# Performance work log

Hardware: AMD Instinct MI355X
Metric: run time of the kernel (lower is better)

Reference implementation:

```python
import jax, jax.numpy as jnp
import numpy as np

DIM = 1024
HEADS = 16
DIM_HEAD = 64
INNER = HEADS * DIM_HEAD  # 1024
EPS = 1e-5


def _layernorm(x, gamma, beta):
    mu = jnp.mean(x, axis=-1, keepdims=True)
    var = jnp.var(x, axis=-1, keepdims=True)
    return (x - mu) * jax.lax.rsqrt(var + EPS) * gamma + beta


def setup_inputs() -> dict:
    key = jax.random.key(0)
    ks = jax.random.split(key, 7)
    b, m, n = 8, 4096, 64
    x = jax.random.normal(ks[0], (b, m, DIM), dtype=jnp.float32)
    latents = jax.random.normal(ks[1], (b, n, DIM), dtype=jnp.float32)
    # LayerNorm params (torch default: weight=1, bias=0; randomize slightly)
    g1 = jnp.ones((DIM,), jnp.float32)
    b1 = jnp.zeros((DIM,), jnp.float32)
    g2 = jnp.ones((DIM,), jnp.float32)
    b2 = jnp.zeros((DIM,), jnp.float32)
    s = 1.0 / np.sqrt(DIM)
    Wq = jax.random.normal(ks[2], (DIM, INNER), jnp.float32) * s   # [in, out]
    Wkv = jax.random.normal(ks[3], (DIM, 2 * INNER), jnp.float32) * s
    Wo = jax.random.normal(ks[4], (INNER, DIM), jnp.float32) * s
    return {"x": x, "latents": latents, "g1": g1, "b1": b1,
            "g2": g2, "b2": b2, "Wq": Wq, "Wkv": Wkv, "Wo": Wo}


def reference(x, latents, g1, b1, g2, b2, Wq, Wkv, Wo):
    b, n, _ = latents.shape
    h, d = HEADS, DIM_HEAD
    scale = d ** -0.5

    xn = _layernorm(x, g1, b1)
    ln = _layernorm(latents, g2, b2)

    q = ln @ Wq                              # [b, n, inner]
    kv_input = jnp.concatenate((xn, ln), axis=1)  # [b, m+n, dim]
    kv = kv_input @ Wkv                      # [b, m+n, 2*inner]
    k, v = jnp.split(kv, 2, axis=-1)
    s_kv = kv_input.shape[1]

    q = q.reshape(b, n, h, d).transpose(0, 2, 1, 3)      # bhnd
    k = k.reshape(b, s_kv, h, d).transpose(0, 2, 1, 3)   # bhsd
    v = v.reshape(b, s_kv, h, d).transpose(0, 2, 1, 3)   # bhsd

    # double-scaling trick: (q*scale) @ (k*scale)^T  => effective 1/d
    weight = jnp.einsum('bhnd,bhsd->bhns', q * scale, k * scale)
    weight = jax.nn.softmax(weight.astype(jnp.float32), axis=-1).astype(weight.dtype)
    out = jnp.einsum('bhns,bhsd->bhnd', weight, v)
    out = out.transpose(0, 2, 1, 3).reshape(b, n, h * d)
    return out @ Wo
```

## Files before the change

### kernel.cpp

```cpp
#include <hip/hip_runtime.h>

typedef __bf16 bf16;
typedef bf16 bf16x4_t __attribute__((ext_vector_type(4)));
typedef bf16 bf16x8_t __attribute__((ext_vector_type(8)));
typedef float f32x4_t __attribute__((ext_vector_type(4)));

#define DI __device__ __forceinline__

DI void gload_lds16(const void* g, void* l) {
  __builtin_amdgcn_global_load_lds((const __attribute__((address_space(1))) void*)g,
                                   (__attribute__((address_space(3))) void*)l, 16, 0, 0);
}

DI f32x4_t mfma16(bf16x8_t a, bf16x8_t b, f32x4_t c) {
  return __builtin_amdgcn_mfma_f32_16x16x32_bf16(a, b, c, 0, 0, 0);
}

DI unsigned short bfbits(float f) {
  bf16 h = (bf16)f;
  return __builtin_bit_cast(unsigned short, h);
}

__global__ __launch_bounds__(256) void prep_all(const float* __restrict__ x,
                                                const float* __restrict__ lat,
                                                const float* __restrict__ g1,
                                                const float* __restrict__ b1,
                                                const float* __restrict__ g2,
                                                const float* __restrict__ b2,
                                                const float* __restrict__ Wq,
                                                const float* __restrict__ Wkv,
                                                const float* __restrict__ Wo,
                                                bf16* __restrict__ kv_in,
                                                bf16* __restrict__ lnq,
                                                bf16* __restrict__ Wq_t,
                                                bf16* __restrict__ Wkv_t,
                                                bf16* __restrict__ Wo_t) {
  const int bid = blockIdx.x;
  const int t = threadIdx.x;
  if (bid < 8320) {
    const int wv = t >> 6, l = t & 63;
    const int row = bid * 4 + wv;
    const float* in;
    const float* gamma;
    const float* beta;
    size_t orow;
    bool dual = false;
    int lrow = 0;
    if (row < 32768) {
      in = x + (size_t)row * 1024;
      gamma = g1; beta = b1;
      orow = (size_t)(row >> 12) * 4160 + (row & 4095);
    } else {
      const int r = row - 32768;
      in = lat + (size_t)r * 1024;
      gamma = g2; beta = b2;
      orow = (size_t)(r >> 6) * 4160 + 4096 + (r & 63);
      dual = true;
      lrow = r;
    }
    float4 v[4];
    float s = 0.f, q = 0.f;
#pragma unroll
    for (int i = 0; i < 4; ++i) {
      v[i] = ((const float4*)in)[i * 64 + l];
      s += v[i].x + v[i].y + v[i].z + v[i].w;
      q += v[i].x * v[i].x + v[i].y * v[i].y + v[i].z * v[i].z + v[i].w * v[i].w;
    }
#pragma unroll
    for (int off = 1; off < 64; off <<= 1) {
      s += __shfl_xor(s, off);
      q += __shfl_xor(q, off);
    }
    const float mu = s * (1.f / 1024.f);
    const float var = q * (1.f / 1024.f) - mu * mu;
    const float rs = rsqrtf(var + 1e-5f);
#pragma unroll
    for (int i = 0; i < 4; ++i) {
      const float4 gv = ((const float4*)gamma)[i * 64 + l];
      const float4 bv = ((const float4*)beta)[i * 64 + l];
      bf16x4_t o;
      o[0] = (bf16)((v[i].x - mu) * rs * gv.x + bv.x);
      o[1] = (bf16)((v[i].y - mu) * rs * gv.y + bv.y);
      o[2] = (bf16)((v[i].z - mu) * rs * gv.z + bv.z);
      o[3] = (bf16)((v[i].w - mu) * rs * gv.w + bv.w);
      *(bf16x4_t*)(kv_in + orow * 1024 + i * 256 + l * 4) = o;
      if (dual) *(bf16x4_t*)(lnq + (size_t)lrow * 1024 + i * 256 + l * 4) = o;
    }
  } else {
    __shared__ float tile[32][33];
    const int b2i = bid - 8320;
    const float* W;
    bf16* Wt;
    int C, t0;
    if (b2i < 1024)      { W = Wq;  Wt = Wq_t;  C = 1024; t0 = b2i; }
    else if (b2i < 3072) { W = Wkv; Wt = Wkv_t; C = 2048; t0 = b2i - 1024; }
    else                 { W = Wo;  Wt = Wo_t;  C = 1024; t0 = b2i - 3072; }
    const int R = 1024;
    const int ntx = C >> 5;
    const int c0 = (t0 % ntx) * 32, r0 = (t0 / ntx) * 32;
    const int tx = t & 31, ty = t >> 5;
#pragma unroll
    for (int j = 0; j < 4; ++j)
      tile[ty + j * 8][tx] = W[(size_t)(r0 + ty + j * 8) * C + c0 + tx];
    __syncthreads();
#pragma unroll
    for (int j = 0; j < 4; ++j)
      Wt[(size_t)(c0 + ty + j * 8) * R + r0 + tx] = (bf16)tile[tx][ty + j * 8];
  }
}

__global__ __launch_bounds__(256) void gemm_bt_sk(const bf16* __restrict__ A,
                                                  const bf16* __restrict__ Bt,
                                                  float* __restrict__ Cf) {
  __shared__ bf16 As[128 * 32];
  __shared__ bf16 Bs[128 * 32];
  const int tid = threadIdx.x;
  const int w = tid >> 6, l = tid & 63;
  const int lg = l >> 4, lr = l & 15;
  const int m0 = blockIdx.y * 128, n0 = blockIdx.x * 128;
  const int kbase = blockIdx.z * 256;
  const int wm = w >> 1, wn = w & 1;
  const int K = 1024, N = 1024;

  f32x4_t acc[4][4];
#pragma unroll
  for (int i = 0; i < 4; ++i)
#pragma unroll
    for (int j = 0; j < 4; ++j)
      acc[i][j] = f32x4_t{0.f, 0.f, 0.f, 0.f};

  for (int kt = 0; kt < 8; ++kt) {
    const int k0 = kbase + kt * 32;
#pragma unroll
    for (int j = 0; j < 2; ++j) {
      const int rb = j * 64 + w * 16;
      const int r = rb + (l >> 2);
      const int c = (l & 3) * 8;
      gload_lds16(A + (size_t)(m0 + r) * K + k0 + c, &As[rb * 32]);
      gload_lds16(Bt + (size_t)(n0 + r) * K + k0 + c, &Bs[rb * 32]);
    }
    __syncthreads();
    bf16x8_t af[4], bfr[4];
#pragma unroll
    for (int i = 0; i < 4; ++i) {
      af[i] = *(const bf16x8_t*)&As[(wm * 64 + i * 16 + lr) * 32 + lg * 8];
      bfr[i] = *(const bf16x8_t*)&Bs[(wn * 64 + i * 16 + lr) * 32 + lg * 8];
    }
#pragma unroll
    for (int mf = 0; mf < 4; ++mf)
#pragma unroll
      for (int nf = 0; nf < 4; ++nf)
        acc[mf][nf] = mfma16(af[mf], bfr[nf], acc[mf][nf]);
    __syncthreads();
  }

#pragma unroll
  for (int mf = 0; mf < 4; ++mf)
#pragma unroll
    for (int r = 0; r < 4; ++r) {
      const int grow = m0 + wm * 64 + mf * 16 + 4 * lg + r;
#pragma unroll
      for (int nf = 0; nf < 4; ++nf) {
        const int gcol = n0 + wn * 64 + nf * 16 + lr;
        unsafeAtomicAdd(&Cf[(size_t)grow * N + gcol], acc[mf][nf][r]);
      }
    }
}

__global__ __launch_bounds__(512, 2) void gemm256_kv(const bf16* __restrict__ Akv,
                                                     const bf16* __restrict__ Aq,
                                                     const bf16* __restrict__ BtKV,
                                                     const bf16* __restrict__ BtQ,
                                                     bf16* __restrict__ Kout,
                                                     bf16* __restrict__ Vout,
                                                     bf16* __restrict__ Qout) {
  extern __shared__ char lds[];
  const int tid = threadIdx.x;
  const int w = tid >> 6, l = tid & 63;
  const int lr = l & 15, lg = l >> 4;
  const int wr = w >> 2, wc = w & 3;

  const int cpx = gridDim.x >> 3;
  const int swz = (blockIdx.x & 7) * cpx + (blockIdx.x >> 3);
  const bool isQ = swz >= 1040;
  const bf16* Ap;
  const bf16* Bp;
  int m0, n0;
  if (!isQ) {
    m0 = (swz >> 3) << 8;
    n0 = (swz & 7) << 8;
    Ap = Akv; Bp = BtKV;
  } else {
    const int qi = swz - 1040;
    m0 = (qi >> 2) << 8;
    n0 = (qi & 3) << 8;
    Ap = Aq; Bp = BtQ;
  }

  auto stage = [&](const bf16* __restrict__ G, int row0, int k0, char* base, int half) {
#pragma unroll
    for (int j = 0; j < 2; ++j) {
      const int r0 = half * 128 + (w * 2 + j) * 8;
      const int row = r0 + (l >> 3);
      const int col = ((l & 7) ^ (l >> 3)) * 8;
      gload_lds16(G + (size_t)(row0 + row) * 1024 + k0 + col, base + r0 * 128);
    }
  };
  auto rdA = [&](char* base, int mf, int ks) -> bf16x8_t {
    const int row = wr * 128 + mf * 16 + lr;
    int byte = row * 128 + (ks * 32 + lg * 8) * 2;
    byte ^= (row & 7) << 4;
    return *(const bf16x8_t*)(base + byte);
  };
  auto rdB = [&](char* base, int nf, int ks) -> bf16x8_t {
    const int row = wc * 64 + nf * 16 + lr;
    int byte = row * 128 + (ks * 32 + lg * 8) * 2;
    byte ^= (row & 7) << 4;
    return *(const bf16x8_t*)(base + byte);
  };

  f32x4_t acc[8][4];
#pragma unroll
  for (int i = 0; i < 8; ++i)
#pragma unroll
    for (int j = 0; j < 4; ++j)
      acc[i][j] = f32x4_t{0.f, 0.f, 0.f, 0.f};

  const int NK = 16;

  stage(Ap, m0, 0, lds, 0);
  stage(Ap, m0, 0, lds, 1);
  stage(Bp, n0, 0, lds + 32768, 0);
  stage(Bp, n0, 0, lds + 32768, 1);
  stage(Ap, m0, 64, lds + 65536, 0);
  stage(Ap, m0, 64, lds + 65536, 1);
  asm volatile("s_waitcnt vmcnt(4)" ::: "memory");
  __builtin_amdgcn_s_barrier();

  bf16x8_t ra[4][2], rb[4][2];
  for (int kt = 0; kt < NK; ++kt) {
    const int cur = kt & 1, nxt = cur ^ 1;
    char* Ac = lds + cur * 65536;
    char* Bc = lds + 32768 + cur * 65536;
    char* Bn = lds + 32768 + nxt * 65536;
    const int k1 = (kt + 1) << 6, k2 = (kt + 2) << 6;

#pragma unroll
    for (int mf = 0; mf < 4; ++mf) { ra[mf][0] = rdA(Ac, mf, 0); ra[mf][1] = rdA(Ac, mf, 1); }
#pragma unroll
    for (int nf = 0; nf < 2; ++nf) { rb[nf][0] = rdB(Bc, nf, 0); rb[nf][1] = rdB(Bc, nf, 1); }
    if (kt + 1 < NK) stage(Bp, n0, k1, Bn, 0);
    asm volatile("s_waitcnt lgkmcnt(0)" ::: "memory");
    __builtin_amdgcn_sched_barrier(0);
    __builtin_amdgcn_s_barrier();
    __builtin_amdgcn_s_setprio(1);
#pragma unroll
    for (int mf = 0; mf < 4; ++mf)
#pragma unroll
      for (int nf = 0; nf < 2; ++nf) {
        acc[mf][nf] = mfma16(ra[mf][0], rb[nf][0], acc[mf][nf]);
        acc[mf][nf] = mfma16(ra[mf][1], rb[nf][1], acc[mf][nf]);
      }
    __builtin_amdgcn_s_setprio(0);

#pragma unroll
    for (int nf = 2; nf < 4; ++nf) { rb[nf][0] = rdB(Bc, nf, 0); rb[nf][1] = rdB(Bc, nf, 1); }
    if (kt + 1 < NK) stage(Bp, n0, k1, Bn, 1);
    asm volatile("s_waitcnt lgkmcnt(0)" ::: "memory");
    __builtin_amdgcn_sched_barrier(0);
    __builtin_amdgcn_s_barrier();
    __builtin_amdgcn_s_setprio(1);
#pragma unroll
    for (int mf = 0; mf < 4; ++mf)
#pragma unroll
      for (int nf = 2; nf < 4; ++nf) {
        acc[mf][nf] = mfma16(ra[mf][0], rb[nf][0], acc[mf][nf]);
        acc[mf][nf] = mfma16(ra[mf][1], rb[nf][1], acc[mf][nf]);
      }
    __builtin_amdgcn_s_setprio(0);

#pragma unroll
    for (int mf = 0; mf < 4; ++mf) { ra[mf][0] = rdA(Ac, mf + 4, 0); ra[mf][1] = rdA(Ac, mf + 4, 1); }
    asm volatile("s_waitcnt lgkmcnt(0)" ::: "memory");
    __builtin_amdgcn_sched_barrier(0);
    __builtin_amdgcn_s_barrier();
    __builtin_amdgcn_s_setprio(1);
#pragma unroll
    for (int mf = 0; mf < 4; ++mf)
#pragma unroll
      for (int nf = 0; nf < 2; ++nf) {
        acc[mf + 4][nf] = mfma16(ra[mf][0], rb[nf][0], acc[mf + 4][nf]);
        acc[mf + 4][nf] = mfma16(ra[mf][1], rb[nf][1], acc[mf + 4][nf]);
      }
    __builtin_amdgcn_s_setprio(0);

    if (kt + 2 < NK) { stage(Ap, m0, k2, Ac, 0); stage(Ap, m0, k2, Ac, 1); }
    if (kt + 2 < NK)
      asm volatile("s_waitcnt vmcnt(4)" ::: "memory");
    else
      asm volatile("s_waitcnt vmcnt(0)" ::: "memory");
    __builtin_amdgcn_sched_barrier(0);
    __builtin_amdgcn_s_barrier();
    __builtin_amdgcn_s_setprio(1);
#pragma unroll
    for (int mf = 0; mf < 4; ++mf)
#pragma unroll
      for (int nf = 2; nf < 4; ++nf) {
        acc[mf + 4][nf] = mfma16(ra[mf][0], rb[nf][0], acc[mf + 4][nf]);
        acc[mf + 4][nf] = mfma16(ra[mf][1], rb[nf][1], acc[mf + 4][nf]);
      }
    __builtin_amdgcn_s_setprio(0);
  }

  if (isQ) {
#pragma unroll
    for (int mf = 0; mf < 8; ++mf) {
      const int grow0 = m0 + wr * 128 + mf * 16 + 4 * lg;
#pragma unroll
      for (int nf = 0; nf < 4; ++nf) {
        const int gcol = n0 + wc * 64 + nf * 16 + lr;
        const int h = gcol >> 6, d = gcol & 63;
#pragma unroll
        for (int r = 0; r < 4; ++r) {
          const int grow = grow0 + r;
          const int b = grow >> 6, i = grow & 63;
          Qout[((size_t)((b * 16 + h) * 64 + i)) * 64 + d] = (bf16)acc[mf][nf][r];
        }
      }
    }
    return;
  }
#pragma unroll
  for (int mf = 0; mf < 8; ++mf) {
    const int grow0 = m0 + wr * 128 + mf * 16 + 4 * lg;
#pragma unroll
    for (int nf = 0; nf < 4; ++nf) {
      const int gcol = n0 + wc * 64 + nf * 16 + lr;
      if (gcol < 1024) {
        const int h = gcol >> 6, d = gcol & 63;
#pragma unroll
        for (int r = 0; r < 4; ++r) {
          const int grow = grow0 + r;
          const int bb = grow / 4160, s = grow % 4160;
          Kout[((size_t)((bb * 16 + h) * 4160 + s)) * 64 + d] = (bf16)acc[mf][nf][r];
        }
      } else {
        const int c2 = gcol - 1024, h = c2 >> 6, d = c2 & 63;
        const int bb = grow0 / 4160, s0 = grow0 % 4160;
        ushort4 u;
        u.x = bfbits(acc[mf][nf][0]);
        u.y = bfbits(acc[mf][nf][1]);
        u.z = bfbits(acc[mf][nf][2]);
        u.w = bfbits(acc[mf][nf][3]);
        *(ushort4*)&Vout[((size_t)((bb * 16 + h) * 64 + d)) * 4160 + s0] = u;
      }
    }
  }
}

__global__ __launch_bounds__(256) void attn_part(const bf16* __restrict__ qb_,
                                                 const bf16* __restrict__ kb_,
                                                 const bf16* __restrict__ vb_,
                                                 float* __restrict__ ob,
                                                 float* __restrict__ mb,
                                                 float* __restrict__ lb) {
  const int c = blockIdx.x;
  const int bh = blockIdx.y;
  const int tid = threadIdx.x;
  const int wave = tid >> 6, l = tid & 63;
  const int lg = l >> 4, lr = l & 15;
  const int qr0 = wave * 16;

  const bf16* q = qb_ + ((size_t)bh * 64 + qr0) * 64;
  const bf16* Kp = kb_ + (size_t)bh * 4160 * 64;
  const bf16* Vt = vb_ + (size_t)bh * 64 * 4160;

  bf16x8_t qf[2];
#pragma unroll
  for (int kk = 0; kk < 2; ++kk)
    qf[kk] = *(const bf16x8_t*)(q + lr * 64 + kk * 32 + lg * 8);

  f32x4_t oacc[4];
  float m[4], lsum[4];
#pragma unroll
  for (int r = 0; r < 4; ++r) { m[r] = -1e30f; lsum[r] = 0.f; }
#pragma unroll
  for (int nf = 0; nf < 4; ++nf) oacc[nf] = f32x4_t{0.f, 0.f, 0.f, 0.f};

  __shared__ bf16 plds[4][16][72];
  bf16(*P)[72] = plds[wave];

  constexpr float inv = 1.0f / 64.0f;

  bf16x8_t kf[2][4];
  auto ldK = [&](int key0) {
#pragma unroll
    for (int kk = 0; kk < 2; ++kk)
#pragma unroll
      for (int nf = 0; nf < 4; ++nf)
        kf[kk][nf] = *(const bf16x8_t*)(Kp + (size_t)(key0 + nf * 16 + lr) * 64 + kk * 32 + lg * 8);
  };

  ldK(c * 832);
  for (int kt = 0; kt < 13; ++kt) {
    const int key0 = c * 832 + kt * 64;
    f32x4_t sf[4];
#pragma unroll
    for (int nf = 0; nf < 4; ++nf) sf[nf] = f32x4_t{0.f, 0.f, 0.f, 0.f};
#pragma unroll
    for (int kk = 0; kk < 2; ++kk)
#pragma unroll
      for (int nf = 0; nf < 4; ++nf)
        sf[nf] = mfma16(qf[kk], kf[kk][nf], sf[nf]);
    if (kt + 1 < 13) ldK(key0 + 64);
    float corr[4];
#pragma unroll
    for (int r = 0; r < 4; ++r) {
      float t = fmaxf(fmaxf(sf[0][r], sf[1][r]), fmaxf(sf[2][r], sf[3][r])) * inv;
#pragma unroll
      for (int off = 1; off < 16; off <<= 1) t = fmaxf(t, __shfl_xor(t, off));
      const float mn = fmaxf(t, m[r]);
      corr[r] = __expf(m[r] - mn);
      m[r] = mn;
    }
    float rowsum[4] = {0.f, 0.f, 0.f, 0.f};
#pragma unroll
    for (int nf = 0; nf < 4; ++nf)
#pragma unroll
      for (int r = 0; r < 4; ++r) {
        const float p = __expf(sf[nf][r] * inv - m[r]);
        rowsum[r] += p;
        P[lg * 4 + r][nf * 16 + lr] = (bf16)p;
      }
#pragma unroll
    for (int r = 0; r < 4; ++r) {
      float t = rowsum[r];
#pragma unroll
      for (int off = 1; off < 16; off <<= 1) t += __shfl_xor(t, off);
      lsum[r] = lsum[r] * corr[r] + t;
    }
#pragma unroll
    for (int nf = 0; nf < 4; ++nf) {
      oacc[nf][0] *= corr[0];
      oacc[nf][1] *= corr[1];
      oacc[nf][2] *= corr[2];
      oacc[nf][3] *= corr[3];
    }
    bf16x8_t vf[2][4];
#pragma unroll
    for (int kk = 0; kk < 2; ++kk)
#pragma unroll
      for (int nf = 0; nf < 4; ++nf)
        vf[kk][nf] = *(const bf16x8_t*)(Vt + (size_t)(nf * 16 + lr) * 4160 + key0 + kk * 32 + lg * 8);
    asm volatile("s_waitcnt lgkmcnt(0)" ::: "memory");
#pragma unroll
    for (int kk = 0; kk < 2; ++kk) {
      bf16x8_t pf = *(const bf16x8_t*)&P[lr][kk * 32 + lg * 8];
#pragma unroll
      for (int nf = 0; nf < 4; ++nf)
        oacc[nf] = mfma16(pf, vf[kk][nf], oacc[nf]);
    }
    asm volatile("s_waitcnt lgkmcnt(0)" ::: "memory");
  }

#pragma unroll
  for (int nf = 0; nf < 4; ++nf)
#pragma unroll
    for (int r = 0; r < 4; ++r) {
      const int i = qr0 + lg * 4 + r;
      ob[((size_t)((bh * 64 + i) * 5 + c)) * 64 + nf * 16 + lr] = oacc[nf][r];
    }
  if (lr == 0) {
#pragma unroll
    for (int r = 0; r < 4; ++r) {
      const int i = qr0 + lg * 4 + r;
      mb[(bh * 64 + i) * 5 + c] = m[r];
      lb[(bh * 64 + i) * 5 + c] = lsum[r];
    }
  }
}

__global__ __launch_bounds__(256) void attn_merge(const float* __restrict__ ob,
                                                  const float* __restrict__ mb,
                                                  const float* __restrict__ lb,
                                                  bf16* __restrict__ aout) {
  const int j = blockIdx.x * 4 + (threadIdx.x >> 6);
  const int l = threadIdx.x & 63;
  float mv[5];
  float mx = -1e30f;
#pragma unroll
  for (int cc = 0; cc < 5; ++cc) { mv[cc] = mb[j * 5 + cc]; mx = fmaxf(mx, mv[cc]); }
  float L = 0.f, o = 0.f;
#pragma unroll
  for (int cc = 0; cc < 5; ++cc) {
    const float wgt = __expf(mv[cc] - mx);
    L += lb[j * 5 + cc] * wgt;
    o += wgt * ob[((size_t)(j * 5 + cc)) * 64 + l];
  }
  const int bh = j >> 6, i = j & 63, b = bh >> 4, h = bh & 15;
  aout[((size_t)(b * 64 + i)) * 1024 + h * 64 + l] = (bf16)(o / L);
}

extern "C" void kernel_launch(void* const* d_in, const int* in_sizes, int n_in,
                              void* d_out, int out_size, void* d_ws, size_t ws_size,
                              hipStream_t stream) {
  (void)in_sizes; (void)n_in; (void)out_size; (void)ws_size;
  const float* x   = (const float*)d_in[0];
  const float* lat = (const float*)d_in[1];
  const float* g1  = (const float*)d_in[2];
  const float* b1  = (const float*)d_in[3];
  const float* g2  = (const float*)d_in[4];
  const float* b2  = (const float*)d_in[5];
  const float* Wq  = (const float*)d_in[6];
  const float* Wkv = (const float*)d_in[7];
  const float* Wo  = (const float*)d_in[8];
  float* out = (float*)d_out;

  char* ws = (char*)d_ws;
  size_t off = 0;
  auto alloc = [&](size_t bytes) {
    void* p = ws + off;
    off += (bytes + 255) & ~(size_t)255;
    return p;
  };
  bf16* kv_in = (bf16*)alloc(8ull * 4160 * 1024 * 2);
  bf16* Wkv_t = (bf16*)alloc(2048ull * 1024 * 2);
  bf16* Wq_t  = (bf16*)alloc(1024ull * 1024 * 2);
  bf16* Wo_t  = (bf16*)alloc(1024ull * 1024 * 2);
  bf16* lnq   = (bf16*)alloc(512ull * 1024 * 2);
  bf16* qbuf  = (bf16*)alloc(512ull * 1024 * 2);
  bf16* kbuf  = (bf16*)alloc(8ull * 16 * 4160 * 64 * 2);
  bf16* vtbuf = (bf16*)alloc(8ull * 16 * 4160 * 64 * 2);
  bf16* aout  = (bf16*)alloc(512ull * 1024 * 2);

  float* obuf = (float*)kv_in;
  float* mbuf = obuf + 8192ull * 5 * 64;
  float* lbuf = mbuf + 8192ull * 5;

  (void)hipFuncSetAttribute(reinterpret_cast<const void*>(gemm256_kv),
                            hipFuncAttributeMaxDynamicSharedMemorySize, 131072);

  prep_all<<<12416, 256, 0, stream>>>(x, lat, g1, b1, g2, b2, Wq, Wkv, Wo,
                                      kv_in, lnq, Wq_t, Wkv_t, Wo_t);

  gemm256_kv<<<1048, 512, 131072, stream>>>(kv_in, lnq, Wkv_t, Wq_t, kbuf, vtbuf, qbuf);

  attn_part<<<dim3(5, 128), 256, 0, stream>>>(qbuf, kbuf, vtbuf, obuf, mbuf, lbuf);
  attn_merge<<<2048, 256, 0, stream>>>(obuf, mbuf, lbuf, aout);

  (void)hipMemsetAsync(out, 0, 512ull * 1024 * 4, stream);
  gemm_bt_sk<<<dim3(8, 4, 4), 256, 0, stream>>>(aout, Wo_t, out);
}
```

Before: 284.5 us.

## Split KV GEMM tail tiles into half-height blocks and fold output memset into merge

The fused KV/Q GEMM is templated on M-fragment count. The last rows of KV tiles are now computed by 128-row blocks (48 extra blocks), which evens out the tail wave across CUs and makes the grid 1072 instead of 1048. The zeroing of the split-K output buffer moves from a separate hipMemsetAsync into attn_merge, removing one launch. This adds template code, a mixed block-size grid and a dependence on attn_merge's grid exactly covering the output buffer.

```diff
diff --git a/kernel.cpp b/kernel.cpp
--- a/kernel.cpp
+++ b/kernel.cpp
@@ -167,47 +167,23 @@
     }
 }
 
-__global__ __launch_bounds__(512, 2) void gemm256_kv(const bf16* __restrict__ Akv,
-                                                     const bf16* __restrict__ Aq,
-                                                     const bf16* __restrict__ BtKV,
-                                                     const bf16* __restrict__ BtQ,
-                                                     bf16* __restrict__ Kout,
-                                                     bf16* __restrict__ Vout,
-                                                     bf16* __restrict__ Qout) {
-  extern __shared__ char lds[];
-  const int tid = threadIdx.x;
-  const int w = tid >> 6, l = tid & 63;
-  const int lr = l & 15, lg = l >> 4;
-  const int wr = w >> 2, wc = w & 3;
-
-  const int cpx = gridDim.x >> 3;
-  const int swz = (blockIdx.x & 7) * cpx + (blockIdx.x >> 3);
-  const bool isQ = swz >= 1040;
-  const bf16* Ap;
-  const bf16* Bp;
-  int m0, n0;
-  if (!isQ) {
-    m0 = (swz >> 3) << 8;
-    n0 = (swz & 7) << 8;
-    Ap = Akv; Bp = BtKV;
-  } else {
-    const int qi = swz - 1040;
-    m0 = (qi >> 2) << 8;
-    n0 = (qi & 3) << 8;
-    Ap = Aq; Bp = BtQ;
-  }
-
-  auto stage = [&](const bf16* __restrict__ G, int row0, int k0, char* base, int half) {
-#pragma unroll
-    for (int j = 0; j < 2; ++j) {
-      const int r0 = half * 128 + (w * 2 + j) * 8;
-      const int row = r0 + (l >> 3);
-      const int col = ((l & 7) ^ (l >> 3)) * 8;
-      gload_lds16(G + (size_t)(row0 + row) * 1024 + k0 + col, base + r0 * 128);
-    }
+template<int MF>
+DI void gemm_body(const bf16* __restrict__ Ap, const bf16* __restrict__ Bp,
+                  int m0, int n0, int mode,
+                  bf16* __restrict__ Kout, bf16* __restrict__ Vout,
+                  bf16* __restrict__ Qout, char* lds,
+                  int w, int l, int lr, int lg, int wr, int wc) {
+  constexpr int ABYTES = MF * 32 * 128;
+  constexpr int AU = MF / 2;
+
+  auto stageU = [&](const bf16* __restrict__ G, int row0, int k0, char* base, int unit) {
+    const int r0 = unit * 64 + w * 8;
+    const int row = r0 + (l >> 3);
+    const int col = ((l & 7) ^ (l >> 3)) * 8;
+    gload_lds16(G + (size_t)(row0 + row) * 1024 + k0 + col, base + r0 * 128);
   };
   auto rdA = [&](char* base, int mf, int ks) -> bf16x8_t {
-    const int row = wr * 128 + mf * 16 + lr;
+    const int row = wr * (MF * 16) + mf * 16 + lr;
     int byte = row * 128 + (ks * 32 + lg * 8) * 2;
     byte ^= (row & 7) << 4;
     return *(const bf16x8_t*)(base + byte);
@@ -219,43 +195,44 @@
     return *(const bf16x8_t*)(base + byte);
   };
 
-  f32x4_t acc[8][4];
-#pragma unroll
-  for (int i = 0; i < 8; ++i)
+  f32x4_t acc[MF][4];
+#pragma unroll
+  for (int i = 0; i < MF; ++i)
 #pragma unroll
     for (int j = 0; j < 4; ++j)
       acc[i][j] = f32x4_t{0.f, 0.f, 0.f, 0.f};
 
   const int NK = 16;
 
-  stage(Ap, m0, 0, lds, 0);
-  stage(Ap, m0, 0, lds, 1);
-  stage(Bp, n0, 0, lds + 32768, 0);
-  stage(Bp, n0, 0, lds + 32768, 1);
-  stage(Ap, m0, 64, lds + 65536, 0);
-  stage(Ap, m0, 64, lds + 65536, 1);
-  asm volatile("s_waitcnt vmcnt(4)" ::: "memory");
+#pragma unroll
+  for (int u = 0; u < AU; ++u) stageU(Ap, m0, 0, lds, u);
+#pragma unroll
+  for (int u = 0; u < 4; ++u) stageU(Bp, n0, 0, lds + ABYTES, u);
+#pragma unroll
+  for (int u = 0; u < AU; ++u) stageU(Ap, m0, 64, lds + ABYTES + 32768, u);
+  if constexpr (MF == 8) asm volatile("s_waitcnt vmcnt(4)" ::: "memory");
+  else                   asm volatile("s_waitcnt vmcnt(2)" ::: "memory");
   __builtin_amdgcn_s_barrier();
 
-  bf16x8_t ra[4][2], rb[4][2];
+  bf16x8_t ra[AU][2], rb[4][2];
   for (int kt = 0; kt < NK; ++kt) {
     const int cur = kt & 1, nxt = cur ^ 1;
-    char* Ac = lds + cur * 65536;
-    char* Bc = lds + 32768 + cur * 65536;
-    char* Bn = lds + 32768 + nxt * 65536;
+    char* Ac = lds + cur * (ABYTES + 32768);
+    char* Bc = Ac + ABYTES;
+    char* Bn = lds + nxt * (ABYTES + 32768) + ABYTES;
     const int k1 = (kt + 1) << 6, k2 = (kt + 2) << 6;
 
 #pragma unroll
-    for (int mf = 0; mf < 4; ++mf) { ra[mf][0] = rdA(Ac, mf, 0); ra[mf][1] = rdA(Ac, mf, 1); }
+    for (int mf = 0; mf < AU; ++mf) { ra[mf][0] = rdA(Ac, mf, 0); ra[mf][1] = rdA(Ac, mf, 1); }
 #pragma unroll
     for (int nf = 0; nf < 2; ++nf) { rb[nf][0] = rdB(Bc, nf, 0); rb[nf][1] = rdB(Bc, nf, 1); }
-    if (kt + 1 < NK) stage(Bp, n0, k1, Bn, 0);
+    if (kt + 1 < NK) { stageU(Bp, n0, k1, Bn, 0); stageU(Bp, n0, k1, Bn, 1); }
     asm volatile("s_waitcnt lgkmcnt(0)" ::: "memory");
     __builtin_amdgcn_sched_barrier(0);
     __builtin_amdgcn_s_barrier();
     __builtin_amdgcn_s_setprio(1);
 #pragma unroll
-    for (int mf = 0; mf < 4; ++mf)
+    for (int mf = 0; mf < AU; ++mf)
 #pragma unroll
       for (int nf = 0; nf < 2; ++nf) {
         acc[mf][nf] = mfma16(ra[mf][0], rb[nf][0], acc[mf][nf]);
@@ -265,13 +242,13 @@
 
 #pragma unroll
     for (int nf = 2; nf < 4; ++nf) { rb[nf][0] = rdB(Bc, nf, 0); rb[nf][1] = rdB(Bc, nf, 1); }
-    if (kt + 1 < NK) stage(Bp, n0, k1, Bn, 1);
+    if (kt + 1 < NK) { stageU(Bp, n0, k1, Bn, 2); stageU(Bp, n0, k1, Bn, 3); }
     asm volatile("s_waitcnt lgkmcnt(0)" ::: "memory");
     __builtin_amdgcn_sched_barrier(0);
     __builtin_amdgcn_s_barrier();
     __builtin_amdgcn_s_setprio(1);
 #pragma unroll
-    for (int mf = 0; mf < 4; ++mf)
+    for (int mf = 0; mf < AU; ++mf)
 #pragma unroll
       for (int nf = 2; nf < 4; ++nf) {
         acc[mf][nf] = mfma16(ra[mf][0], rb[nf][0], acc[mf][nf]);
@@ -280,42 +257,45 @@
     __builtin_amdgcn_s_setprio(0);
 
 #pragma unroll
-    for (int mf = 0; mf < 4; ++mf) { ra[mf][0] = rdA(Ac, mf + 4, 0); ra[mf][1] = rdA(Ac, mf + 4, 1); }
+    for (int mf = 0; mf < AU; ++mf) { ra[mf][0] = rdA(Ac, mf + AU, 0); ra[mf][1] = rdA(Ac, mf + AU, 1); }
     asm volatile("s_waitcnt lgkmcnt(0)" ::: "memory");
     __builtin_amdgcn_sched_barrier(0);
     __builtin_amdgcn_s_barrier();
     __builtin_amdgcn_s_setprio(1);
 #pragma unroll
-    for (int mf = 0; mf < 4; ++mf)
+    for (int mf = 0; mf < AU; ++mf)
 #pragma unroll
       for (int nf = 0; nf < 2; ++nf) {
-        acc[mf + 4][nf] = mfma16(ra[mf][0], rb[nf][0], acc[mf + 4][nf]);
-        acc[mf + 4][nf] = mfma16(ra[mf][1], rb[nf][1], acc[mf + 4][nf]);
+        acc[mf + AU][nf] = mfma16(ra[mf][0], rb[nf][0], acc[mf + AU][nf]);
+        acc[mf + AU][nf] = mfma16(ra[mf][1], rb[nf][1], acc[mf + AU][nf]);
       }
     __builtin_amdgcn_s_setprio(0);
 
-    if (kt + 2 < NK) { stage(Ap, m0, k2, Ac, 0); stage(Ap, m0, k2, Ac, 1); }
-    if (kt + 2 < NK)
-      asm volatile("s_waitcnt vmcnt(4)" ::: "memory");
-    else
+    if (kt + 2 < NK) {
+#pragma unroll
+      for (int u = 0; u < AU; ++u) stageU(Ap, m0, k2, Ac, u);
+      if constexpr (MF == 8) asm volatile("s_waitcnt vmcnt(4)" ::: "memory");
+      else                   asm volatile("s_waitcnt vmcnt(2)" ::: "memory");
+    } else {
       asm volatile("s_waitcnt vmcnt(0)" ::: "memory");
+    }
     __builtin_amdgcn_sched_barrier(0);
     __builtin_amdgcn_s_barrier();
     __builtin_amdgcn_s_setprio(1);
 #pragma unroll
-    for (int mf = 0; mf < 4; ++mf)
+    for (int mf = 0; mf < AU; ++mf)
 #pragma unroll
       for (int nf = 2; nf < 4; ++nf) {
-        acc[mf + 4][nf] = mfma16(ra[mf][0], rb[nf][0], acc[mf + 4][nf]);
-        acc[mf + 4][nf] = mfma16(ra[mf][1], rb[nf][1], acc[mf + 4][nf]);
+        acc[mf + AU][nf] = mfma16(ra[mf][0], rb[nf][0], acc[mf + AU][nf]);
+        acc[mf + AU][nf] = mfma16(ra[mf][1], rb[nf][1], acc[mf + AU][nf]);
       }
     __builtin_amdgcn_s_setprio(0);
   }
 
-  if (isQ) {
-#pragma unroll
-    for (int mf = 0; mf < 8; ++mf) {
-      const int grow0 = m0 + wr * 128 + mf * 16 + 4 * lg;
+  if (mode == 1) {
+#pragma unroll
+    for (int mf = 0; mf < MF; ++mf) {
+      const int grow0 = m0 + wr * (MF * 16) + mf * 16 + 4 * lg;
 #pragma unroll
       for (int nf = 0; nf < 4; ++nf) {
         const int gcol = n0 + wc * 64 + nf * 16 + lr;
@@ -331,8 +311,8 @@
     return;
   }
 #pragma unroll
-  for (int mf = 0; mf < 8; ++mf) {
-    const int grow0 = m0 + wr * 128 + mf * 16 + 4 * lg;
+  for (int mf = 0; mf < MF; ++mf) {
+    const int grow0 = m0 + wr * (MF * 16) + mf * 16 + 4 * lg;
 #pragma unroll
     for (int nf = 0; nf < 4; ++nf) {
       const int gcol = n0 + wc * 64 + nf * 16 + lr;
@@ -358,6 +338,39 @@
   }
 }
 
+__global__ __launch_bounds__(512, 2) void gemm256_kv(const bf16* __restrict__ Akv,
+                                                     const bf16* __restrict__ Aq,
+                                                     const bf16* __restrict__ BtKV,
+                                                     const bf16* __restrict__ BtQ,
+                                                     bf16* __restrict__ Kout,
+                                                     bf16* __restrict__ Vout,
+                                                     bf16* __restrict__ Qout) {
+  extern __shared__ char lds[];
+  const int tid = threadIdx.x;
+  const int w = tid >> 6, l = tid & 63;
+  const int lr = l & 15, lg = l >> 4;
+  const int wr = w >> 2, wc = w & 3;
+  const int bid = blockIdx.x;
+
+  if (bid < 1024) {
+    const int swz = (bid & 7) * 128 + (bid >> 3);
+    if (swz < 1016) {
+      const int m0 = (swz >> 3) << 8, n0 = (swz & 7) << 8;
+      gemm_body<8>(Akv, BtKV, m0, n0, 0, Kout, Vout, Qout, lds, w, l, lr, lg, wr, wc);
+    } else {
+      const int qi = swz - 1016;
+      const int m0 = (qi >> 2) << 8, n0 = (qi & 3) << 8;
+      gemm_body<8>(Aq, BtQ, m0, n0, 1, Kout, Vout, Qout, lds, w, l, lr, lg, wr, wc);
+    }
+  } else {
+    const int h2 = bid - 1024;
+    const int t = h2 >> 1;
+    const int tm = 127 + t / 8, tn = t % 8;
+    const int m0 = tm * 256 + (h2 & 1) * 128;
+    gemm_body<4>(Akv, BtKV, m0, tn << 8, 0, Kout, Vout, Qout, lds, w, l, lr, lg, wr, wc);
+  }
+}
+
 __global__ __launch_bounds__(256) void attn_part(const bf16* __restrict__ qb_,
                                                  const bf16* __restrict__ kb_,
                                                  const bf16* __restrict__ vb_,
@@ -483,7 +496,10 @@
 __global__ __launch_bounds__(256) void attn_merge(const float* __restrict__ ob,
                                                   const float* __restrict__ mb,
                                                   const float* __restrict__ lb,
-                                                  bf16* __restrict__ aout) {
+                                                  bf16* __restrict__ aout,
+                                                  float* __restrict__ outz) {
+  outz[(size_t)blockIdx.x * 256 + threadIdx.x] = 0.f;
+
   const int j = blockIdx.x * 4 + (threadIdx.x >> 6);
   const int l = threadIdx.x & 63;
   float mv[5];
@@ -543,11 +559,10 @@
   prep_all<<<12416, 256, 0, stream>>>(x, lat, g1, b1, g2, b2, Wq, Wkv, Wo,
                                       kv_in, lnq, Wq_t, Wkv_t, Wo_t);
 
-  gemm256_kv<<<1048, 512, 131072, stream>>>(kv_in, lnq, Wkv_t, Wq_t, kbuf, vtbuf, qbuf);
+  gemm256_kv<<<1072, 512, 131072, stream>>>(kv_in, lnq, Wkv_t, Wq_t, kbuf, vtbuf, qbuf);
 
   attn_part<<<dim3(5, 128), 256, 0, stream>>>(qbuf, kbuf, vtbuf, obuf, mbuf, lbuf);
-  attn_merge<<<2048, 256, 0, stream>>>(obuf, mbuf, lbuf, aout);
-
-  (void)hipMemsetAsync(out, 0, 512ull * 1024 * 4, stream);
+  attn_merge<<<2048, 256, 0, stream>>>(obuf, mbuf, lbuf, aout, out);
+
   gemm_bt_sk<<<dim3(8, 4, 4), 256, 0, stream>>>(aout, Wo_t, out);
 }
```

Result: faster. 273.2 us (-4.0%).
